# Optimization experiments

Measured on AMD Instinct MI355X. Metric: run time of the kernel, lower is better.

The kernel has to match this reference:

```python
import jax, jax.numpy as jnp
import numpy as np

DIM = 2048
N_HEADS = 16
N_KV_HEADS = 4
HEAD_DIM = DIM // N_HEADS  # 128
N_REP = N_HEADS // N_KV_HEADS
EPS = 1e-6


def rmsnorm(x, w):
    norm = jax.lax.rsqrt(jnp.mean(x * x, axis=-1, keepdims=True) + EPS)
    return x * norm * w


def apply_rope(xq, xk, freqs_cis):
    # xq: (B,S,Hq,D), xk: (B,S,Hk,D); freqs_cis: (S, D/2, 2) -> (cos, sin)
    cos = freqs_cis[None, :, None, :, 0]  # (1,S,1,D/2)
    sin = freqs_cis[None, :, None, :, 1]

    def rot(x):
        xr = x.reshape(*x.shape[:-1], HEAD_DIM // 2, 2)
        x0, x1 = xr[..., 0], xr[..., 1]
        o0 = x0 * cos - x1 * sin
        o1 = x0 * sin + x1 * cos
        return jnp.stack([o0, o1], axis=-1).reshape(x.shape)

    return rot(xq), rot(xk)


def setup_inputs() -> dict:
    key = jax.random.key(0)
    k1, k2, k3, k4, k5, k6 = jax.random.split(key, 6)
    B, S = 2, 2048
    x = jax.random.normal(k1, (B, S, DIM), dtype=jnp.float32)
    x_mask = jnp.ones((B, S), dtype=bool)
    freqs_cis = jax.random.uniform(k2, (S, HEAD_DIM // 2, 2), dtype=jnp.float32)
    qkv_out = (N_HEADS + 2 * N_KV_HEADS) * HEAD_DIM  # 3072
    w_qkv = jax.random.normal(k3, (qkv_out, DIM), dtype=jnp.float32) * (DIM ** -0.5)
    w_out = jax.random.normal(k4, (DIM, N_HEADS * HEAD_DIM), dtype=jnp.float32) * (DIM ** -0.5)
    qn_w = jnp.ones((HEAD_DIM,), dtype=jnp.float32)
    kn_w = jnp.ones((HEAD_DIM,), dtype=jnp.float32)
    return {"x": x, "x_mask": x_mask, "freqs_cis": freqs_cis,
            "w_qkv": w_qkv, "w_out": w_out, "qn_w": qn_w, "kn_w": kn_w}


def reference(x, x_mask, freqs_cis, w_qkv, w_out, qn_w, kn_w):
    B, S, _ = x.shape
    qkv = x @ w_qkv.T  # (B,S,3072)
    dq = N_HEADS * HEAD_DIM
    dkv = N_KV_HEADS * HEAD_DIM
    xq = qkv[..., :dq].reshape(B, S, N_HEADS, HEAD_DIM)
    xk = qkv[..., dq:dq + dkv].reshape(B, S, N_KV_HEADS, HEAD_DIM)
    xv = qkv[..., dq + dkv:].reshape(B, S, N_KV_HEADS, HEAD_DIM)
    xq = rmsnorm(xq, qn_w)
    xk = rmsnorm(xk, kn_w)
    xq, xk = apply_rope(xq, xk, freqs_cis)
    # GQA: repeat kv heads
    xk = jnp.repeat(xk, N_REP, axis=2)  # (B,S,H,D)
    xv = jnp.repeat(xv, N_REP, axis=2)
    # SDPA: (B,H,S,D)
    q = jnp.moveaxis(xq, 1, 2)
    k = jnp.moveaxis(xk, 1, 2)
    v = jnp.moveaxis(xv, 1, 2)
    scale = HEAD_DIM ** -0.5
    scores = jnp.einsum('bhqd,bhkd->bhqk', q, k) * scale
    bias = jnp.where(x_mask[:, None, None, :], 0.0, -jnp.inf).astype(q.dtype)
    attn = jax.nn.softmax(scores + bias, axis=-1)
    out = jnp.einsum('bhqk,bhkd->bhqd', attn, v)
    out = jnp.moveaxis(out, 1, 2).reshape(B, S, N_HEADS * HEAD_DIM)
    return out @ w_out.T
```

## Files before the change

kernel.cpp:

```cpp
#include <hip/hip_runtime.h>
#include <hip/hip_bf16.h>

#define DIMSZ 2048
#define SLEN  2048
#define NH    16
#define NKV   4
#define HD    128
#define NTOK  4096
#define QKVN  3072

typedef __bf16 bf16x8 __attribute__((ext_vector_type(8)));
typedef __bf16 bf16x4 __attribute__((ext_vector_type(4)));
typedef short  s16x4  __attribute__((ext_vector_type(4)));
typedef float  floatx4 __attribute__((ext_vector_type(4)));

__device__ __forceinline__ void async16(const __bf16* g, __bf16* l) {
    __builtin_amdgcn_global_load_lds(
        (const __attribute__((address_space(1))) void*)g,
        (__attribute__((address_space(3))) void*)l, 16, 0, 0);
}

__device__ __forceinline__ floatx4 mfma16x16x16_bf16(s16x4 a, s16x4 b, floatx4 c) {
#if __has_builtin(__builtin_amdgcn_mfma_f32_16x16x16bf16_1k)
    return __builtin_amdgcn_mfma_f32_16x16x16bf16_1k(a, b, c, 0, 0, 0);
#else
    asm volatile("v_mfma_f32_16x16x16_bf16 %0, %1, %2, %0"
                 : "+v"(c) : "v"(a), "v"(b));
    return c;
#endif
}

__global__ __launch_bounds__(256) void cvt_f32_bf16(const float* __restrict__ src,
                                                    __bf16* __restrict__ dst, int n) {
    int i = (blockIdx.x * 256 + threadIdx.x) * 8;
    if (i >= n) return;
    float4 a = *(const float4*)(src + i);
    float4 b = *(const float4*)(src + i + 4);
    bf16x8 o;
    o[0] = (__bf16)a.x; o[1] = (__bf16)a.y; o[2] = (__bf16)a.z; o[3] = (__bf16)a.w;
    o[4] = (__bf16)b.x; o[5] = (__bf16)b.y; o[6] = (__bf16)b.z; o[7] = (__bf16)b.w;
    *(bf16x8*)(dst + i) = o;
}

template <typename CT>
__global__ __launch_bounds__(256) void gemm_bt(const __bf16* __restrict__ A,
                                               const __bf16* __restrict__ B,
                                               CT* __restrict__ C,
                                               int M, int N, int K) {
    __shared__ __align__(16) __bf16 As[128 * 64];
    __shared__ __align__(16) __bf16 Bs[128 * 64];
    const int tid  = threadIdx.x;
    const int wave = tid >> 6, lane = tid & 63;
    const int lr = lane & 15, lq = lane >> 4;
    const int wm = (wave >> 1) * 64, wn = (wave & 1) * 64;
    const int tm0 = blockIdx.y * 128, tn0 = blockIdx.x * 128;

    floatx4 acc[4][4] = {};

    for (int k0 = 0; k0 < K; k0 += 64) {
#pragma unroll
        for (int i = 0; i < 4; ++i) {
            int c   = tid + 256 * i;
            int row = c >> 3, col = (c & 7) * 8;
            async16(&A[(size_t)(tm0 + row) * K + k0 + col], &As[c * 8]);
            async16(&B[(size_t)(tn0 + row) * K + k0 + col], &Bs[c * 8]);
        }
        __syncthreads();
#pragma unroll
        for (int kk = 0; kk < 2; ++kk) {
            bf16x8 af[4], bg[4];
#pragma unroll
            for (int i = 0; i < 4; ++i)
                af[i] = *(const bf16x8*)&As[(wm + i * 16 + lr) * 64 + kk * 32 + lq * 8];
#pragma unroll
            for (int j = 0; j < 4; ++j)
                bg[j] = *(const bf16x8*)&Bs[(wn + j * 16 + lr) * 64 + kk * 32 + lq * 8];
#pragma unroll
            for (int i = 0; i < 4; ++i)
#pragma unroll
                for (int j = 0; j < 4; ++j)
                    acc[i][j] = __builtin_amdgcn_mfma_f32_16x16x32_bf16(
                        af[i], bg[j], acc[i][j], 0, 0, 0);
        }
        __syncthreads();
    }
#pragma unroll
    for (int i = 0; i < 4; ++i)
#pragma unroll
        for (int j = 0; j < 4; ++j)
#pragma unroll
            for (int r = 0; r < 4; ++r) {
                int row = tm0 + wm + i * 16 + lq * 4 + r;
                int col = tn0 + wn + j * 16 + lr;
                C[(size_t)row * N + col] = (CT)acc[i][j][r];
            }
}

__global__ __launch_bounds__(256) void norm_rope(const __bf16* __restrict__ qkv,
                                                 const float* __restrict__ freqs,
                                                 const float* __restrict__ qn_w,
                                                 const float* __restrict__ kn_w,
                                                 __bf16* __restrict__ Qo,
                                                 __bf16* __restrict__ Ko) {
    const int tok = blockIdx.x * 4 + (threadIdx.x >> 6);
    const int hd  = blockIdx.y;
    const int t   = threadIdx.x & 63;
    const int s   = tok & (SLEN - 1);
    const int b   = tok >> 11;
    const bool isq = hd < NH;
    const int h    = isq ? hd : hd - NH;
    const int base = isq ? h * HD : (NH * HD + h * HD);

    const __bf16* src = qkv + (size_t)tok * QKVN + base + 2 * t;
    float x0 = (float)src[0], x1 = (float)src[1];
    float ss = x0 * x0 + x1 * x1;
#pragma unroll
    for (int off = 32; off >= 1; off >>= 1) ss += __shfl_xor(ss, off);
    float rs = rsqrtf(ss * (1.0f / 128.0f) + 1e-6f);

    const float* w = isq ? qn_w : kn_w;
    float w0 = w[2 * t], w1 = w[2 * t + 1];
    float cs = freqs[(s * 64 + t) * 2 + 0];
    float sn = freqs[(s * 64 + t) * 2 + 1];
    float n0 = x0 * rs * w0, n1 = x1 * rs * w1;
    float o0 = n0 * cs - n1 * sn;
    float o1 = n0 * sn + n1 * cs;
    if (isq) { o0 *= 0.08838834764831845f; o1 *= 0.08838834764831845f; }

    __bf16* dst = isq ? (Qo + (((size_t)(b * NH + h)) * SLEN + s) * HD + 2 * t)
                      : (Ko + (((size_t)(b * NKV + h)) * SLEN + s) * HD + 2 * t);
    dst[0] = (__bf16)o0;
    dst[1] = (__bf16)o1;
}

__global__ __launch_bounds__(256) void v_transpose(const __bf16* __restrict__ qkv,
                                                   __bf16* __restrict__ VT) {
    __shared__ __align__(16) __bf16 L[64 * 136];
    const int st  = blockIdx.x;
    const int kh  = blockIdx.y;
    const int b   = blockIdx.z;
    const int tid = threadIdx.x;
#pragma unroll
    for (int i = 0; i < 4; ++i) {
        int c = tid + 256 * i;
        int srow = c >> 4, dc = (c & 15) * 8;
        int tok = b * SLEN + st * 64 + srow;
        *(int4*)&L[srow * 136 + dc] =
            *(const int4*)&qkv[(size_t)tok * QKVN + 2560 + kh * HD + dc];
    }
    __syncthreads();
#pragma unroll
    for (int i = 0; i < 4; ++i) {
        int c = tid + 256 * i;
        int d = c >> 3, sc = (c & 7) * 8;
        __bf16 tmp[8];
#pragma unroll
        for (int j = 0; j < 8; ++j) tmp[j] = L[(sc + j) * 136 + d];
        *(int4*)&VT[(((size_t)(b * NKV + kh)) * HD + d) * SLEN + st * 64 + sc] =
            *(int4*)tmp;
    }
}

__global__ __launch_bounds__(256) void attn(const __bf16* __restrict__ Q,
                                            const __bf16* __restrict__ Kn,
                                            const __bf16* __restrict__ VT,
                                            __bf16* __restrict__ O) {
    __shared__ __align__(16) __bf16 Ks [2][64 * 128];
    __shared__ __align__(16) __bf16 Vts[2][128 * 64];
    const int qt  = blockIdx.x;
    const int h   = blockIdx.y;
    const int b   = blockIdx.z;
    const int tid = threadIdx.x;
    const int w = tid >> 6, lane = tid & 63, lr = lane & 15, lq = lane >> 4;
    const int kh = h >> 2;

    const __bf16* Qb = Q  + ((size_t)(b * NH + h))   * SLEN * HD;
    const __bf16* Kb = Kn + ((size_t)(b * NKV + kh)) * SLEN * HD;
    const __bf16* Vb = VT + ((size_t)(b * NKV + kh)) * HD * SLEN;

    bf16x8 qf[2][4];
    const int qbase = qt * 128 + w * 32;
#pragma unroll
    for (int g2 = 0; g2 < 2; ++g2)
#pragma unroll
        for (int kc = 0; kc < 4; ++kc)
            qf[g2][kc] = *(const bf16x8*)
                &Qb[(size_t)(qbase + g2 * 16 + lr) * HD + kc * 32 + lq * 8];

    floatx4 oacc[2][8] = {};
    float l_i[2] = {0.f, 0.f};

    auto stage = [&](int buf, int kt) {
#pragma unroll
        for (int i = 0; i < 4; ++i) {
            int c = tid + 256 * i;
            int row = c >> 4, u = c & 15;
            int g = u ^ (row & 7);
            async16(&Kb[(size_t)(kt * 64 + row) * HD + g * 8], &Ks[buf][c * 8]);
        }
#pragma unroll
        for (int i = 0; i < 4; ++i) {
            int c = tid + 256 * i;
            int d = c >> 3, u = c & 7;
            int g = u ^ (d & 7);
            async16(&Vb[(size_t)d * SLEN + kt * 64 + g * 8], &Vts[buf][c * 8]);
        }
    };

    stage(0, 0);
    for (int kt = 0; kt < 32; ++kt) {
        const int buf = kt & 1;
        __syncthreads();
        if (kt < 31) stage(buf ^ 1, kt + 1);

        floatx4 sacc[2][4] = {};
#pragma unroll
        for (int nt = 0; nt < 4; ++nt)
#pragma unroll
            for (int kc = 0; kc < 4; ++kc) {
                bf16x8 kf = *(const bf16x8*)
                    &Ks[buf][(nt * 16 + lr) * 128 + ((kc * 4 + lq) ^ (lr & 7)) * 8];
                sacc[0][nt] = __builtin_amdgcn_mfma_f32_16x16x32_bf16(
                    kf, qf[0][kc], sacc[0][nt], 0, 0, 0);
                sacc[1][nt] = __builtin_amdgcn_mfma_f32_16x16x32_bf16(
                    kf, qf[1][kc], sacc[1][nt], 0, 0, 0);
            }

        s16x4 pf[2][4];
#pragma unroll
        for (int g2 = 0; g2 < 2; ++g2) {
            float rsum = 0.f;
#pragma unroll
            for (int nt = 0; nt < 4; ++nt) {
                bf16x4 pb;
#pragma unroll
                for (int r = 0; r < 4; ++r) {
                    float p = __expf(sacc[g2][nt][r]);
                    rsum += p;
                    pb[r] = (__bf16)p;
                }
                pf[g2][nt] = *(s16x4*)&pb;
            }
            l_i[g2] += rsum;
        }

#pragma unroll
        for (int dt = 0; dt < 8; ++dt)
#pragma unroll
            for (int nt = 0; nt < 4; ++nt) {
                int u = (2 * nt + (lq >> 1)) ^ (lr & 7);
                s16x4 vf = *(const s16x4*)
                    &Vts[buf][(dt * 16 + lr) * 64 + u * 8 + (lq & 1) * 4];
                oacc[0][dt] = mfma16x16x16_bf16(vf, pf[0][nt], oacc[0][dt]);
                oacc[1][dt] = mfma16x16x16_bf16(vf, pf[1][nt], oacc[1][dt]);
            }
    }

#pragma unroll
    for (int g2 = 0; g2 < 2; ++g2) {
        float l = l_i[g2];
        l += __shfl_xor(l, 16);
        l += __shfl_xor(l, 32);
        float inv = 1.0f / l;
        int qs = qbase + g2 * 16 + lr;
        __bf16* orow = O + (((size_t)(b * SLEN + qs)) * NH + h) * HD;
#pragma unroll
        for (int dt = 0; dt < 8; ++dt) {
            bf16x4 ob;
#pragma unroll
            for (int r = 0; r < 4; ++r) ob[r] = (__bf16)(oacc[g2][dt][r] * inv);
            *(bf16x4*)&orow[dt * 16 + lq * 4] = ob;
        }
    }
}

extern "C" void kernel_launch(void* const* d_in, const int* in_sizes, int n_in,
                              void* d_out, int out_size, void* d_ws, size_t ws_size,
                              hipStream_t stream) {
    const float* x     = (const float*)d_in[0];
    const float* freqs = (const float*)d_in[2];
    const float* w_qkv = (const float*)d_in[3];
    const float* w_out = (const float*)d_in[4];
    const float* qn_w  = (const float*)d_in[5];
    const float* kn_w  = (const float*)d_in[6];
    float* out = (float*)d_out;

    char* ws = (char*)d_ws;
    __bf16* qkv = (__bf16*)ws;
    __bf16* Qb  = (__bf16*)(ws + 25165824ull);
    __bf16* Kb  = (__bf16*)(ws + 25165824ull + 16777216);
    __bf16* VTb = (__bf16*)(ws + 25165824ull + 16777216 + 4194304);
    __bf16* xb  = (__bf16*)(ws + 50331648ull);
    __bf16* wqb = (__bf16*)(ws + 50331648ull + 16777216);
    __bf16* wob = (__bf16*)(ws + 50331648ull + 16777216 + 12582912);
    __bf16* Ob  = (__bf16*)ws;

    cvt_f32_bf16<<<NTOK * DIMSZ / 2048, 256, 0, stream>>>(x, xb, NTOK * DIMSZ);
    cvt_f32_bf16<<<QKVN * DIMSZ / 2048, 256, 0, stream>>>(w_qkv, wqb, QKVN * DIMSZ);
    cvt_f32_bf16<<<DIMSZ * DIMSZ / 2048, 256, 0, stream>>>(w_out, wob, DIMSZ * DIMSZ);

    gemm_bt<__bf16><<<dim3(QKVN / 128, NTOK / 128), 256, 0, stream>>>(
        xb, wqb, qkv, NTOK, QKVN, DIMSZ);

    norm_rope<<<dim3(NTOK / 4, NH + NKV), 256, 0, stream>>>(qkv, freqs, qn_w, kn_w, Qb, Kb);
    v_transpose<<<dim3(32, NKV, 2), 256, 0, stream>>>(qkv, VTb);

    attn<<<dim3(SLEN / 128, NH, 2), 256, 0, stream>>>(Qb, Kb, VTb, Ob);

    gemm_bt<float><<<dim3(DIMSZ / 128, NTOK / 128), 256, 0, stream>>>(
        Ob, wob, out, NTOK, DIMSZ, DIMSZ);
}
```

Baseline: 369.4 us.

## Double-buffer GEMM LDS tiles and merge conversion and prep launches

The GEMM kernel now uses two LDS buffers, so the async global-to-LDS load of the next K tile is issued while the current tile is multiplied, with one barrier per iteration instead of two. The three fp32-to-bf16 conversion launches are merged into one kernel that picks its source by block index, and norm/rope and the V transpose are merged into a single prep launch. This targets exposed load latency in the GEMMs and per-launch overhead. The cost is double the LDS per GEMM block, which may lower occupancy, plus extra branching and idle blocks in the merged prep kernel.

```diff
diff --git a/kernel.cpp b/kernel.cpp
--- a/kernel.cpp
+++ b/kernel.cpp
@@ -30,16 +30,22 @@
 #endif
 }
 
-__global__ __launch_bounds__(256) void cvt_f32_bf16(const float* __restrict__ src,
-                                                    __bf16* __restrict__ dst, int n) {
-    int i = (blockIdx.x * 256 + threadIdx.x) * 8;
-    if (i >= n) return;
-    float4 a = *(const float4*)(src + i);
-    float4 b = *(const float4*)(src + i + 4);
+__global__ __launch_bounds__(256) void cvt3(const float* __restrict__ s0, __bf16* __restrict__ d0, int n0,
+                                            const float* __restrict__ s1, __bf16* __restrict__ d1, int n1,
+                                            const float* __restrict__ s2, __bf16* __restrict__ d2, int n2) {
+    int blk = blockIdx.x;
+    int b0 = n0 >> 11, b1 = n1 >> 11;
+    const float* s; __bf16* d; int base;
+    if (blk < b0)           { s = s0; d = d0; base = blk << 11; }
+    else if (blk < b0 + b1) { s = s1; d = d1; base = (blk - b0) << 11; }
+    else                    { s = s2; d = d2; base = (blk - b0 - b1) << 11; }
+    int i = base + threadIdx.x * 8;
+    float4 a = *(const float4*)(s + i);
+    float4 b = *(const float4*)(s + i + 4);
     bf16x8 o;
     o[0] = (__bf16)a.x; o[1] = (__bf16)a.y; o[2] = (__bf16)a.z; o[3] = (__bf16)a.w;
     o[4] = (__bf16)b.x; o[5] = (__bf16)b.y; o[6] = (__bf16)b.z; o[7] = (__bf16)b.w;
-    *(bf16x8*)(dst + i) = o;
+    *(bf16x8*)(d + i) = o;
 }
 
 template <typename CT>
@@ -47,8 +53,8 @@
                                                const __bf16* __restrict__ B,
                                                CT* __restrict__ C,
                                                int M, int N, int K) {
-    __shared__ __align__(16) __bf16 As[128 * 64];
-    __shared__ __align__(16) __bf16 Bs[128 * 64];
+    __shared__ __align__(16) __bf16 As[2][128 * 64];
+    __shared__ __align__(16) __bf16 Bs[2][128 * 64];
     const int tid  = threadIdx.x;
     const int wave = tid >> 6, lane = tid & 63;
     const int lr = lane & 15, lq = lane >> 4;
@@ -57,24 +63,31 @@
 
     floatx4 acc[4][4] = {};
 
-    for (int k0 = 0; k0 < K; k0 += 64) {
+    auto stage = [&](int buf, int k0) {
 #pragma unroll
         for (int i = 0; i < 4; ++i) {
             int c   = tid + 256 * i;
             int row = c >> 3, col = (c & 7) * 8;
-            async16(&A[(size_t)(tm0 + row) * K + k0 + col], &As[c * 8]);
-            async16(&B[(size_t)(tn0 + row) * K + k0 + col], &Bs[c * 8]);
-        }
+            async16(&A[(size_t)(tm0 + row) * K + k0 + col], &As[buf][c * 8]);
+            async16(&B[(size_t)(tn0 + row) * K + k0 + col], &Bs[buf][c * 8]);
+        }
+    };
+
+    const int nIter = K >> 6;
+    stage(0, 0);
+    for (int it = 0; it < nIter; ++it) {
+        const int buf = it & 1;
         __syncthreads();
+        if (it + 1 < nIter) stage(buf ^ 1, (it + 1) << 6);
 #pragma unroll
         for (int kk = 0; kk < 2; ++kk) {
             bf16x8 af[4], bg[4];
 #pragma unroll
             for (int i = 0; i < 4; ++i)
-                af[i] = *(const bf16x8*)&As[(wm + i * 16 + lr) * 64 + kk * 32 + lq * 8];
+                af[i] = *(const bf16x8*)&As[buf][(wm + i * 16 + lr) * 64 + kk * 32 + lq * 8];
 #pragma unroll
             for (int j = 0; j < 4; ++j)
-                bg[j] = *(const bf16x8*)&Bs[(wn + j * 16 + lr) * 64 + kk * 32 + lq * 8];
+                bg[j] = *(const bf16x8*)&Bs[buf][(wn + j * 16 + lr) * 64 + kk * 32 + lq * 8];
 #pragma unroll
             for (int i = 0; i < 4; ++i)
 #pragma unroll
@@ -82,7 +95,6 @@
                     acc[i][j] = __builtin_amdgcn_mfma_f32_16x16x32_bf16(
                         af[i], bg[j], acc[i][j], 0, 0, 0);
         }
-        __syncthreads();
     }
 #pragma unroll
     for (int i = 0; i < 4; ++i)
@@ -96,68 +108,69 @@
             }
 }
 
-__global__ __launch_bounds__(256) void norm_rope(const __bf16* __restrict__ qkv,
-                                                 const float* __restrict__ freqs,
-                                                 const float* __restrict__ qn_w,
-                                                 const float* __restrict__ kn_w,
-                                                 __bf16* __restrict__ Qo,
-                                                 __bf16* __restrict__ Ko) {
-    const int tok = blockIdx.x * 4 + (threadIdx.x >> 6);
-    const int hd  = blockIdx.y;
-    const int t   = threadIdx.x & 63;
-    const int s   = tok & (SLEN - 1);
-    const int b   = tok >> 11;
-    const bool isq = hd < NH;
-    const int h    = isq ? hd : hd - NH;
-    const int base = isq ? h * HD : (NH * HD + h * HD);
-
-    const __bf16* src = qkv + (size_t)tok * QKVN + base + 2 * t;
-    float x0 = (float)src[0], x1 = (float)src[1];
-    float ss = x0 * x0 + x1 * x1;
-#pragma unroll
-    for (int off = 32; off >= 1; off >>= 1) ss += __shfl_xor(ss, off);
-    float rs = rsqrtf(ss * (1.0f / 128.0f) + 1e-6f);
-
-    const float* w = isq ? qn_w : kn_w;
-    float w0 = w[2 * t], w1 = w[2 * t + 1];
-    float cs = freqs[(s * 64 + t) * 2 + 0];
-    float sn = freqs[(s * 64 + t) * 2 + 1];
-    float n0 = x0 * rs * w0, n1 = x1 * rs * w1;
-    float o0 = n0 * cs - n1 * sn;
-    float o1 = n0 * sn + n1 * cs;
-    if (isq) { o0 *= 0.08838834764831845f; o1 *= 0.08838834764831845f; }
-
-    __bf16* dst = isq ? (Qo + (((size_t)(b * NH + h)) * SLEN + s) * HD + 2 * t)
-                      : (Ko + (((size_t)(b * NKV + h)) * SLEN + s) * HD + 2 * t);
-    dst[0] = (__bf16)o0;
-    dst[1] = (__bf16)o1;
-}
-
-__global__ __launch_bounds__(256) void v_transpose(const __bf16* __restrict__ qkv,
-                                                   __bf16* __restrict__ VT) {
-    __shared__ __align__(16) __bf16 L[64 * 136];
-    const int st  = blockIdx.x;
-    const int kh  = blockIdx.y;
-    const int b   = blockIdx.z;
-    const int tid = threadIdx.x;
-#pragma unroll
-    for (int i = 0; i < 4; ++i) {
-        int c = tid + 256 * i;
-        int srow = c >> 4, dc = (c & 15) * 8;
-        int tok = b * SLEN + st * 64 + srow;
-        *(int4*)&L[srow * 136 + dc] =
-            *(const int4*)&qkv[(size_t)tok * QKVN + 2560 + kh * HD + dc];
-    }
-    __syncthreads();
-#pragma unroll
-    for (int i = 0; i < 4; ++i) {
-        int c = tid + 256 * i;
-        int d = c >> 3, sc = (c & 7) * 8;
-        __bf16 tmp[8];
-#pragma unroll
-        for (int j = 0; j < 8; ++j) tmp[j] = L[(sc + j) * 136 + d];
-        *(int4*)&VT[(((size_t)(b * NKV + kh)) * HD + d) * SLEN + st * 64 + sc] =
-            *(int4*)tmp;
+__global__ __launch_bounds__(256) void prep(const __bf16* __restrict__ qkv,
+                                            const float* __restrict__ freqs,
+                                            const float* __restrict__ qn_w,
+                                            const float* __restrict__ kn_w,
+                                            __bf16* __restrict__ Qo,
+                                            __bf16* __restrict__ Ko,
+                                            __bf16* __restrict__ VT) {
+    if (blockIdx.y < 20) {
+        const int tok = blockIdx.x * 4 + (threadIdx.x >> 6);
+        const int hd  = blockIdx.y;
+        const int t   = threadIdx.x & 63;
+        const int s   = tok & (SLEN - 1);
+        const int b   = tok >> 11;
+        const bool isq = hd < NH;
+        const int h    = isq ? hd : hd - NH;
+        const int base = isq ? h * HD : (NH * HD + h * HD);
+
+        const __bf16* src = qkv + (size_t)tok * QKVN + base + 2 * t;
+        float x0 = (float)src[0], x1 = (float)src[1];
+        float ss = x0 * x0 + x1 * x1;
+#pragma unroll
+        for (int off = 32; off >= 1; off >>= 1) ss += __shfl_xor(ss, off);
+        float rs = rsqrtf(ss * (1.0f / 128.0f) + 1e-6f);
+
+        const float* w = isq ? qn_w : kn_w;
+        float w0 = w[2 * t], w1 = w[2 * t + 1];
+        float cs = freqs[(s * 64 + t) * 2 + 0];
+        float sn = freqs[(s * 64 + t) * 2 + 1];
+        float n0 = x0 * rs * w0, n1 = x1 * rs * w1;
+        float o0 = n0 * cs - n1 * sn;
+        float o1 = n0 * sn + n1 * cs;
+        if (isq) { o0 *= 0.08838834764831845f; o1 *= 0.08838834764831845f; }
+
+        __bf16* dst = isq ? (Qo + (((size_t)(b * NH + h)) * SLEN + s) * HD + 2 * t)
+                          : (Ko + (((size_t)(b * NKV + h)) * SLEN + s) * HD + 2 * t);
+        dst[0] = (__bf16)o0;
+        dst[1] = (__bf16)o1;
+    } else {
+        if (blockIdx.x >= 256) return;
+        __shared__ __align__(16) __bf16 L[64 * 136];
+        const int kh  = blockIdx.x >> 6;
+        const int b   = (blockIdx.x >> 5) & 1;
+        const int st  = blockIdx.x & 31;
+        const int tid = threadIdx.x;
+#pragma unroll
+        for (int i = 0; i < 4; ++i) {
+            int c = tid + 256 * i;
+            int srow = c >> 4, dc = (c & 15) * 8;
+            int tok = b * SLEN + st * 64 + srow;
+            *(int4*)&L[srow * 136 + dc] =
+                *(const int4*)&qkv[(size_t)tok * QKVN + 2560 + kh * HD + dc];
+        }
+        __syncthreads();
+#pragma unroll
+        for (int i = 0; i < 4; ++i) {
+            int c = tid + 256 * i;
+            int d = c >> 3, sc = (c & 7) * 8;
+            __bf16 tmp[8];
+#pragma unroll
+            for (int j = 0; j < 8; ++j) tmp[j] = L[(sc + j) * 136 + d];
+            *(int4*)&VT[(((size_t)(b * NKV + kh)) * HD + d) * SLEN + st * 64 + sc] =
+                *(int4*)tmp;
+        }
     }
 }
 
@@ -295,15 +308,13 @@
     __bf16* wob = (__bf16*)(ws + 50331648ull + 16777216 + 12582912);
     __bf16* Ob  = (__bf16*)ws;
 
-    cvt_f32_bf16<<<NTOK * DIMSZ / 2048, 256, 0, stream>>>(x, xb, NTOK * DIMSZ);
-    cvt_f32_bf16<<<QKVN * DIMSZ / 2048, 256, 0, stream>>>(w_qkv, wqb, QKVN * DIMSZ);
-    cvt_f32_bf16<<<DIMSZ * DIMSZ / 2048, 256, 0, stream>>>(w_out, wob, DIMSZ * DIMSZ);
+    cvt3<<<dim3((NTOK * DIMSZ + QKVN * DIMSZ + DIMSZ * DIMSZ) / 2048), 256, 0, stream>>>(
+        x, xb, NTOK * DIMSZ, w_qkv, wqb, QKVN * DIMSZ, w_out, wob, DIMSZ * DIMSZ);
 
     gemm_bt<__bf16><<<dim3(QKVN / 128, NTOK / 128), 256, 0, stream>>>(
         xb, wqb, qkv, NTOK, QKVN, DIMSZ);
 
-    norm_rope<<<dim3(NTOK / 4, NH + NKV), 256, 0, stream>>>(qkv, freqs, qn_w, kn_w, Qb, Kb);
-    v_transpose<<<dim3(32, NKV, 2), 256, 0, stream>>>(qkv, VTb);
+    prep<<<dim3(NTOK / 4, 21), 256, 0, stream>>>(qkv, freqs, qn_w, kn_w, Qb, Kb, VTb);
 
     attn<<<dim3(SLEN / 128, NH, 2), 256, 0, stream>>>(Qb, Kb, VTb, Ob);
 
```

After: 357.5 us. -3.2%, faster.
